# Performance work log

Hardware: AMD Instinct MI355X
Metric: run time of the kernel (lower is better)

Reference implementation:

```python
import jax, jax.numpy as jnp
import numpy as np


def setup_inputs() -> dict:
    key = jax.random.key(0)
    x = jax.random.normal(key, (8388608, 9), dtype=jnp.float32)
    return {"x": x}


def reference(x):
    # x[..., 0:9] is a row-major flattened 3x3 matrix F:
    #   [a b c; d e f; g h i]  -> det via cofactor expansion (same math as
    #   torch.linalg.det on the stacked 3x3, but closed-form).
    a, b, c = x[..., 0], x[..., 1], x[..., 2]
    d, e, f = x[..., 3], x[..., 4], x[..., 5]
    g, h, i = x[..., 6], x[..., 7], x[..., 8]
    det = a * (e * i - f * h) - b * (d * i - f * g) + c * (d * h - e * g)
    return det[..., None]  # unsqueeze(-1), shape [..., 1]
```

## Files before the change

### kernel.cpp

```cpp
#include <hip/hip_runtime.h>


#define TPB 256
#define ROWS_PER_BLOCK 256
#define FLOATS_PER_TILE (ROWS_PER_BLOCK * 9)
#define VEC4_PER_TILE (FLOATS_PER_TILE / 4)

__global__ __launch_bounds__(TPB) void det3_kernel(const float* __restrict__ x,
                                                   float* __restrict__ out,
                                                   long long n) {
    __shared__ float s[FLOATS_PER_TILE];
    const int tid = threadIdx.x;
    const long long row0 = (long long)blockIdx.x * ROWS_PER_BLOCK;

    if (row0 + ROWS_PER_BLOCK <= n) {
        const float4* g4 = reinterpret_cast<const float4*>(x + row0 * 9);
        float4* s4 = reinterpret_cast<float4*>(s);
        s4[tid] = g4[tid];
        s4[tid + 256] = g4[tid + 256];
        if (tid < VEC4_PER_TILE - 512) s4[tid + 512] = g4[tid + 512];
    } else {
        const long long base = row0 * 9;
        const long long limit = n * 9;
        for (int j = tid; j < FLOATS_PER_TILE; j += TPB) {
            const long long gi = base + j;
            s[j] = (gi < limit) ? x[gi] : 0.0f;
        }
    }
    __syncthreads();

    const long long row = row0 + tid;
    if (row < n) {
        const float* m = &s[tid * 9];
        const float a = m[0], b = m[1], c = m[2];
        const float d = m[3], e = m[4], f = m[5];
        const float g = m[6], h = m[7], i = m[8];
        const float det = a * (e * i - f * h)
                        - b * (d * i - f * g)
                        + c * (d * h - e * g);
        out[row] = det;
    }
}

extern "C" void kernel_launch(void* const* d_in, const int* in_sizes, int n_in,
                              void* d_out, int out_size, void* d_ws, size_t ws_size,
                              hipStream_t stream) {
    const float* x = (const float*)d_in[0];
    float* out = (float*)d_out;
    const long long n = (long long)in_sizes[0] / 9;
    const int blocks = (int)((n + ROWS_PER_BLOCK - 1) / ROWS_PER_BLOCK);
    det3_kernel<<<blocks, TPB, 0, stream>>>(x, out, n);
}
```

Baseline: 62.04 us.

## Process four rows per thread with vectorized LDS reads and float4 nontemporal stores

Each thread now handles four consecutive 3x3 matrices, so each block covers 1024 rows and the grid is four times smaller. The thread reads its 36 floats from shared memory as nine float4 loads, computes four determinants and writes them as one nontemporal float4 store. The goal is fewer blocks, wider global stores and vector LDS reads in place of scalar ones, which may help this bandwidth-bound kernel. Shared memory per block rises to 36 KB, which can lower occupancy, and the 144-byte per-thread stride in LDS may cause bank conflicts.

```diff
diff --git a/kernel.cpp b/kernel.cpp
--- a/kernel.cpp
+++ b/kernel.cpp
@@ -1,10 +1,12 @@
 #include <hip/hip_runtime.h>
 
 
+typedef float fx4 __attribute__((ext_vector_type(4)));
+
 #define TPB 256
-#define ROWS_PER_BLOCK 256
+#define ROWS_PER_THREAD 4
+#define ROWS_PER_BLOCK (TPB * ROWS_PER_THREAD)
 #define FLOATS_PER_TILE (ROWS_PER_BLOCK * 9)
-#define VEC4_PER_TILE (FLOATS_PER_TILE / 4)
 
 __global__ __launch_bounds__(TPB) void det3_kernel(const float* __restrict__ x,
                                                    float* __restrict__ out,
@@ -14,31 +16,53 @@
     const long long row0 = (long long)blockIdx.x * ROWS_PER_BLOCK;
 
     if (row0 + ROWS_PER_BLOCK <= n) {
-        const float4* g4 = reinterpret_cast<const float4*>(x + row0 * 9);
-        float4* s4 = reinterpret_cast<float4*>(s);
-        s4[tid] = g4[tid];
-        s4[tid + 256] = g4[tid + 256];
-        if (tid < VEC4_PER_TILE - 512) s4[tid + 512] = g4[tid + 512];
+        const fx4* __restrict__ g4 = reinterpret_cast<const fx4*>(x + row0 * 9);
+        fx4* s4 = reinterpret_cast<fx4*>(s);
+#pragma unroll
+        for (int k = 0; k < 9; ++k) {
+            s4[tid + k * TPB] = g4[tid + k * TPB];
+        }
+        __syncthreads();
+
+        fx4 q[9];
+        const fx4* sv = reinterpret_cast<const fx4*>(&s[tid * 36]);
+#pragma unroll
+        for (int k = 0; k < 9; ++k) q[k] = sv[k];
+        const float* m = reinterpret_cast<const float*>(q);
+
+        fx4 r;
+#pragma unroll
+        for (int rrow = 0; rrow < ROWS_PER_THREAD; ++rrow) {
+            const float* mm = m + rrow * 9;
+            const float a = mm[0], b = mm[1], c = mm[2];
+            const float d = mm[3], e = mm[4], f = mm[5];
+            const float g = mm[6], h = mm[7], i = mm[8];
+            r[rrow] = a * (e * i - f * h)
+                    - b * (d * i - f * g)
+                    + c * (d * h - e * g);
+        }
+        fx4* out4 = reinterpret_cast<fx4*>(out + row0);
+        __builtin_nontemporal_store(r, &out4[tid]);
     } else {
-        const long long base = row0 * 9;
         const long long limit = n * 9;
         for (int j = tid; j < FLOATS_PER_TILE; j += TPB) {
-            const long long gi = base + j;
+            const long long gi = row0 * 9 + j;
             s[j] = (gi < limit) ? x[gi] : 0.0f;
         }
-    }
-    __syncthreads();
-
-    const long long row = row0 + tid;
-    if (row < n) {
-        const float* m = &s[tid * 9];
-        const float a = m[0], b = m[1], c = m[2];
-        const float d = m[3], e = m[4], f = m[5];
-        const float g = m[6], h = m[7], i = m[8];
-        const float det = a * (e * i - f * h)
-                        - b * (d * i - f * g)
-                        + c * (d * h - e * g);
-        out[row] = det;
+        __syncthreads();
+#pragma unroll
+        for (int rrow = 0; rrow < ROWS_PER_THREAD; ++rrow) {
+            const long long row = row0 + (long long)tid * ROWS_PER_THREAD + rrow;
+            if (row < n) {
+                const float* mm = &s[(tid * ROWS_PER_THREAD + rrow) * 9];
+                const float a = mm[0], b = mm[1], c = mm[2];
+                const float d = mm[3], e = mm[4], f = mm[5];
+                const float g = mm[6], h = mm[7], i = mm[8];
+                out[row] = a * (e * i - f * h)
+                         - b * (d * i - f * g)
+                         + c * (d * h - e * g);
+            }
+        }
     }
 }
 
```

After: 55.78 us. 10.1% less time.
